# Kernel tuning notes

Hardware: AMD Instinct MI355X
Metric: run time of the kernel (lower is better)

The kernel has to match this reference:

```python
import jax, jax.numpy as jnp
import numpy as np
from jax import lax

B, T, K = 2048, 1024, 8  # batch, max seq len, num_tags


def setup_inputs() -> dict:
    key = jax.random.key(0)
    k1, k2, k3, k4, k5, k6, k7 = jax.random.split(key, 7)
    score = jax.random.normal(k1, (B, T, K), jnp.float32)
    log_p = jax.nn.log_softmax(jax.random.normal(k2, (B, T, K), jnp.float32), axis=-1)
    tags = jax.random.randint(k3, (B, T), 0, K)
    seq_l = jax.random.randint(k4, (B,), 1, T + 1)  # valid lengths in [1, T]
    transitions = jax.random.normal(k5, (K, K), jnp.float32) * 0.1
    start_transitions = jax.random.normal(k6, (K,), jnp.float32) * 0.1
    end_transitions = jax.random.normal(k7, (K,), jnp.float32) * 0.1
    return {
        "log_p": log_p,
        "score": score,
        "transitions": transitions,
        "start_transitions": start_transitions,
        "end_transitions": end_transitions,
        "tags": tags,
        "seq_l": seq_l,
    }


def _crf_nll(score, tags, mask, transitions, start_transitions, end_transitions):
    """Linear-chain CRF negative log-likelihood, summed over the batch.
    score: [B,T,K] emissions; tags: [B,T] gold; mask: [B,T] bool."""
    maskf = mask.astype(score.dtype)

    # ---- numerator: score of the gold tag path ----
    emit = jnp.take_along_axis(score, tags[..., None], axis=-1)[..., 0]  # [B,T]
    num = (emit * maskf).sum(-1)
    num = num + start_transitions[tags[:, 0]]
    trans_sc = transitions[tags[:, :-1], tags[:, 1:]]  # [B,T-1]
    num = num + (trans_sc * maskf[:, 1:]).sum(-1)
    last_idx = (mask.sum(-1).astype(jnp.int32) - 1)  # [B]
    last_tag = jnp.take_along_axis(tags, last_idx[:, None], axis=1)[:, 0]
    num = num + end_transitions[last_tag]

    # ---- denominator: log partition via log-sum-exp scan over time ----
    alpha0 = start_transitions[None, :] + score[:, 0]  # [B,K]

    def step(alpha, xs):
        emit_t, mask_t = xs  # [B,K], [B]
        # alpha[b,i] + transitions[i,j] + emit[b,j], logsumexp over i
        nxt = jax.nn.logsumexp(alpha[:, :, None] + transitions[None, :, :], axis=1) + emit_t
        alpha = jnp.where(mask_t[:, None], nxt, alpha)  # freeze past end-of-seq
        return alpha, None

    xs = (jnp.swapaxes(score[:, 1:], 0, 1), jnp.swapaxes(mask[:, 1:], 0, 1))
    alpha, _ = lax.scan(step, alpha0, xs)
    log_z = jax.nn.logsumexp(alpha + end_transitions[None, :], axis=-1)  # [B]

    return -(num - log_z).sum()


def reference(log_p, score, transitions, start_transitions, end_transitions, tags, seq_l):
    mask = jnp.arange(T)[None, :] < seq_l[:, None]  # [B,T] bool
    loss = _crf_nll(score, tags, mask, transitions, start_transitions, end_transitions) / B
    # training path: quick predictions = argmax over per-token log_p, zero-padded
    pred_idx = jnp.argmax(log_p, axis=-1) * mask.astype(jnp.int64)
    return loss, pred_idx
```

## Files before the change

### kernel.cpp

```cpp
#include <hip/hip_runtime.h>
#include <hip/hip_bf16.h>


namespace {

constexpr int B = 2048;
constexpr int T = 1024;

__device__ __forceinline__ float max8(const float* a) {
  return fmaxf(fmaxf(fmaxf(a[0], a[1]), fmaxf(a[2], a[3])),
               fmaxf(fmaxf(a[4], a[5]), fmaxf(a[6], a[7])));
}

__global__ __launch_bounds__(256) void pred_num_kernel(
    const float* __restrict__ log_p, const float* __restrict__ score,
    const float* __restrict__ trans, const float* __restrict__ start_tr,
    const float* __restrict__ end_tr, const int* __restrict__ tags,
    const int* __restrict__ seq_l, float* __restrict__ out_pred,
    float* __restrict__ ws_num) {
  int tid = blockIdx.x * blockDim.x + threadIdx.x;
  int g0 = tid << 2;
  int b = g0 >> 10;
  int t0 = g0 & (T - 1);
  int L = seq_l[b];

  const float4* lp = reinterpret_cast<const float4*>(log_p) + (g0 << 1);
  float4 u[8];
#pragma unroll
  for (int r = 0; r < 8; ++r) u[r] = lp[r];
  int4 tg4 = *reinterpret_cast<const int4*>(tags + g0);
  int tg[4] = {tg4.x, tg4.y, tg4.z, tg4.w};
  int prev0 = (t0 == 0) ? 0 : tags[g0 - 1];

  float contrib = 0.0f;
#pragma unroll
  for (int r = 0; r < 4; ++r) {
    float v[8] = {u[2 * r].x, u[2 * r].y, u[2 * r].z, u[2 * r].w,
                  u[2 * r + 1].x, u[2 * r + 1].y, u[2 * r + 1].z,
                  u[2 * r + 1].w};
    int best = 0;
    float bv = v[0];
#pragma unroll
    for (int j = 1; j < 8; ++j) {
      if (v[j] > bv) { bv = v[j]; best = j; }
    }
    int t = t0 + r;
    bool act = (t < L);
    out_pred[g0 + r] = act ? (float)best : 0.0f;
    if (act) {
      int tgr = tg[r];
      float csum = score[(size_t)(g0 + r) * 8 + tgr];
      if (t == 0)
        csum += start_tr[tgr];
      else
        csum += trans[((r == 0) ? prev0 : tg[r - 1]) * 8 + tgr];
      if (t == L - 1) csum += end_tr[tgr];
      contrib += csum;
    }
  }
#pragma unroll
  for (int off = 32; off >= 1; off >>= 1) contrib += __shfl_down(contrib, off);
  if ((threadIdx.x & 63) == 0) atomicAdd(&ws_num[b], contrib);
}

template <int NC, int LOG_NC>
__global__ __launch_bounds__(256) void chunk_kernel(
    const float* __restrict__ score, const float* __restrict__ trans,
    const int* __restrict__ seq_l, float* __restrict__ wsA,
    float* __restrict__ wsS) {
  constexpr int CL = T / NC;
  int g = blockIdx.x * blockDim.x + threadIdx.x;
  int k = g & 7;
  int c = (g >> 3) & (NC - 1);
  int b = g >> (3 + LOG_NC);

  float E[8][8];
#pragma unroll
  for (int i = 0; i < 8; ++i)
#pragma unroll
    for (int j = 0; j < 8; ++j) E[i][j] = __expf(trans[i * 8 + j]);

  float a[8];
#pragma unroll
  for (int j = 0; j < 8; ++j) a[j] = (j == k) ? 1.0f : 0.0f;
  float sig = 0.0f;

  int L = seq_l[b];
  int t0 = c * CL;
  int ts = (c == 0) ? 1 : t0;
  int te = min(t0 + CL, L);
  int n = te - ts;
  const float* sp = score + ((size_t)b * T + ts) * 8;

  float4 nA, nB;
  if (n > 0) {
    nA = *reinterpret_cast<const float4*>(sp);
    nB = *reinterpret_cast<const float4*>(sp + 4);
  }
  for (int it = 0; it < n; ++it) {
    float4 sA = nA, sB = nB;
    if (it + 1 < n) {
      nA = *reinterpret_cast<const float4*>(sp + 8);
      nB = *reinterpret_cast<const float4*>(sp + 12);
    }
    sp += 8;
    float em[8] = {__expf(sA.x), __expf(sA.y), __expf(sA.z), __expf(sA.w),
                   __expf(sB.x), __expf(sB.y), __expf(sB.z), __expf(sB.w)};
    float na[8];
#pragma unroll
    for (int j = 0; j < 8; ++j) {
      float acc = E[0][j] * a[0];
#pragma unroll
      for (int i = 1; i < 8; ++i) acc = fmaf(E[i][j], a[i], acc);
      na[j] = em[j] * acc;
    }
#pragma unroll
    for (int j = 0; j < 8; ++j) a[j] = na[j];
    if ((it & 7) == 7) {
      float mm = max8(a);
      float r = __builtin_amdgcn_rcpf(mm);
#pragma unroll
      for (int j = 0; j < 8; ++j) a[j] *= r;
      sig += __logf(mm);
    }
  }
  {
    float mm = max8(a);
    if (mm > 0.0f) {
      float r = __builtin_amdgcn_rcpf(mm);
#pragma unroll
      for (int j = 0; j < 8; ++j) a[j] *= r;
      sig += __logf(mm);
    }
  }

  float* Ao = wsA + (size_t)(b * NC + c) * 64;
#pragma unroll
  for (int j = 0; j < 8; ++j) Ao[j * 8 + k] = a[j];
  wsS[(b * NC + c) * 8 + k] = sig;
}

template <int NC>
__global__ __launch_bounds__(256) void combine_kernel(
    const float* __restrict__ score, const float* __restrict__ start_tr,
    const float* __restrict__ end_tr, const float* __restrict__ wsA,
    const float* __restrict__ wsS, const float* __restrict__ ws_num,
    float* __restrict__ out_loss) {
  int tid = blockIdx.x * blockDim.x + threadIdx.x;
  int j = tid & 7;
  int b = tid >> 3;

  float pj = __expf(start_tr[j] + score[(size_t)b * T * 8 + j]);
  float mm = pj;
#pragma unroll
  for (int m = 1; m < 8; m <<= 1) mm = fmaxf(mm, __shfl_xor(mm, m, 8));
  float tau = __logf(mm);
  pj *= __builtin_amdgcn_rcpf(mm);

  float eej = __expf(end_tr[j]);

  const float* Ab = wsA + (size_t)b * NC * 64;
  const float* Sb = wsS + (size_t)b * NC * 8;
  float4 r0 = *reinterpret_cast<const float4*>(Ab + j * 8);
  float4 r1 = *reinterpret_cast<const float4*>(Ab + j * 8 + 4);
  float sgj = Sb[j];

  for (int c = 0; c < NC; ++c) {
    float4 c0 = r0, c1 = r1;
    float sj = sgj;
    if (c + 1 < NC) {
      const float* An = Ab + (size_t)(c + 1) * 64;
      r0 = *reinterpret_cast<const float4*>(An + j * 8);
      r1 = *reinterpret_cast<const float4*>(An + j * 8 + 4);
      sgj = Sb[(c + 1) * 8 + j];
    }
    float smax = sj;
#pragma unroll
    for (int m = 1; m < 8; m <<= 1) smax = fmaxf(smax, __shfl_xor(smax, m, 8));
    float wj = pj * __expf(sj - smax);
    float w[8];
#pragma unroll
    for (int i = 0; i < 8; ++i) w[i] = __shfl(wj, i, 8);
    float acc = c0.x * w[0];
    acc = fmaf(c0.y, w[1], acc);
    acc = fmaf(c0.z, w[2], acc);
    acc = fmaf(c0.w, w[3], acc);
    acc = fmaf(c1.x, w[4], acc);
    acc = fmaf(c1.y, w[5], acc);
    acc = fmaf(c1.z, w[6], acc);
    acc = fmaf(c1.w, w[7], acc);
    float mm2 = acc;
#pragma unroll
    for (int m = 1; m < 8; m <<= 1) mm2 = fmaxf(mm2, __shfl_xor(mm2, m, 8));
    tau += smax + __logf(mm2);
    pj = acc * __builtin_amdgcn_rcpf(mm2);
  }

  float term = pj * eej;
#pragma unroll
  for (int m = 1; m < 8; m <<= 1) term += __shfl_xor(term, m, 8);
  float logz = tau + __logf(term);

  float part = (j == 0) ? (logz - ws_num[b]) * (1.0f / (float)B) : 0.0f;
#pragma unroll
  for (int off = 32; off >= 1; off >>= 1) part += __shfl_down(part, off);
  if ((threadIdx.x & 63) == 0) atomicAdd(out_loss, part);
}

}

extern "C" void kernel_launch(void* const* d_in, const int* in_sizes, int n_in,
                              void* d_out, int out_size, void* d_ws,
                              size_t ws_size, hipStream_t stream) {
  const float* log_p = (const float*)d_in[0];
  const float* score = (const float*)d_in[1];
  const float* trans = (const float*)d_in[2];
  const float* start_tr = (const float*)d_in[3];
  const float* end_tr = (const float*)d_in[4];
  const int* tags = (const int*)d_in[5];
  const int* seq_l = (const int*)d_in[6];
  float* out = (float*)d_out;

  size_t need64 = ((size_t)B * 64 * 72 + B) * sizeof(float);
  bool use64 = ws_size >= need64;

  int nc = use64 ? 64 : 32;
  float* wsA = (float*)d_ws;
  float* wsS = wsA + (size_t)B * nc * 64;
  float* wsNum = wsS + (size_t)B * nc * 8;

  hipMemsetAsync(wsNum, 0, B * sizeof(float), stream);
  hipMemsetAsync(out, 0, sizeof(float), stream);

  pred_num_kernel<<<(B * T / 4) / 256, 256, 0, stream>>>(
      log_p, score, trans, start_tr, end_tr, tags, seq_l, out + 1, wsNum);
  if (use64) {
    chunk_kernel<64, 6><<<(B * 64 * 8) / 256, 256, 0, stream>>>(
        score, trans, seq_l, wsA, wsS);
    combine_kernel<64><<<(B * 8) / 256, 256, 0, stream>>>(
        score, start_tr, end_tr, wsA, wsS, wsNum, out);
  } else {
    chunk_kernel<32, 5><<<(B * 32 * 8) / 256, 256, 0, stream>>>(
        score, trans, seq_l, wsA, wsS);
    combine_kernel<32><<<(B * 8) / 256, 256, 0, stream>>>(
        score, start_tr, end_tr, wsA, wsS, wsNum, out);
  }
}
```

Baseline: 236.7 us.

## Balance CRF chunks by sequence length, use persistent work queue and tree combine

Chunks are now sized by each sequence's valid length, so every chunk does similar work and no chunk runs past the end of a sequence. A persistent grid pulls tasks from an atomic counter. Score loads are cooperative float4 reads, with the emissions spread to lanes by shuffles. The serial per-batch combine over 64 chunks becomes a log-depth tree reduction of transfer matrices in shared memory, one block per batch. The exp of the transition matrix is computed once in an init kernel, which also replaces the memsets, and the workspace-size fallback is removed, so the workspace must be large enough.

```diff
diff --git a/kernel.cpp b/kernel.cpp
--- a/kernel.cpp
+++ b/kernel.cpp
@@ -6,10 +6,23 @@
 
 constexpr int B = 2048;
 constexpr int T = 1024;
+constexpr int NC = 64;
+constexpr int NTASK = B * (NC / 8);
 
 __device__ __forceinline__ float max8(const float* a) {
   return fmaxf(fmaxf(fmaxf(a[0], a[1]), fmaxf(a[2], a[3])),
                fmaxf(fmaxf(a[4], a[5]), fmaxf(a[6], a[7])));
+}
+
+__global__ void init_kernel(const float* __restrict__ trans,
+                            float* __restrict__ expE,
+                            float* __restrict__ ws_num, int* __restrict__ ctr,
+                            float* __restrict__ out0) {
+  int i = threadIdx.x;
+  for (int r = i; r < B; r += 256) ws_num[r] = 0.0f;
+  if (i < 64) expE[i] = __expf(trans[i]);
+  if (i == 64) *ctr = 0;
+  if (i == 65) *out0 = 0.0f;
 }
 
 __global__ __launch_bounds__(256) void pred_num_kernel(
@@ -63,148 +76,191 @@
   if ((threadIdx.x & 63) == 0) atomicAdd(&ws_num[b], contrib);
 }
 
-template <int NC, int LOG_NC>
 __global__ __launch_bounds__(256) void chunk_kernel(
-    const float* __restrict__ score, const float* __restrict__ trans,
+    const float* __restrict__ score, const float* __restrict__ expE,
     const int* __restrict__ seq_l, float* __restrict__ wsA,
-    float* __restrict__ wsS) {
-  constexpr int CL = T / NC;
-  int g = blockIdx.x * blockDim.x + threadIdx.x;
-  int k = g & 7;
-  int c = (g >> 3) & (NC - 1);
-  int b = g >> (3 + LOG_NC);
-
-  float E[8][8];
-#pragma unroll
-  for (int i = 0; i < 8; ++i)
-#pragma unroll
-    for (int j = 0; j < 8; ++j) E[i][j] = __expf(trans[i * 8 + j]);
-
-  float a[8];
-#pragma unroll
-  for (int j = 0; j < 8; ++j) a[j] = (j == k) ? 1.0f : 0.0f;
-  float sig = 0.0f;
-
-  int L = seq_l[b];
-  int t0 = c * CL;
-  int ts = (c == 0) ? 1 : t0;
-  int te = min(t0 + CL, L);
-  int n = te - ts;
-  const float* sp = score + ((size_t)b * T + ts) * 8;
-
-  float4 nA, nB;
-  if (n > 0) {
-    nA = *reinterpret_cast<const float4*>(sp);
-    nB = *reinterpret_cast<const float4*>(sp + 4);
-  }
-  for (int it = 0; it < n; ++it) {
-    float4 sA = nA, sB = nB;
-    if (it + 1 < n) {
-      nA = *reinterpret_cast<const float4*>(sp + 8);
-      nB = *reinterpret_cast<const float4*>(sp + 12);
-    }
-    sp += 8;
-    float em[8] = {__expf(sA.x), __expf(sA.y), __expf(sA.z), __expf(sA.w),
-                   __expf(sB.x), __expf(sB.y), __expf(sB.z), __expf(sB.w)};
-    float na[8];
-#pragma unroll
-    for (int j = 0; j < 8; ++j) {
-      float acc = E[0][j] * a[0];
-#pragma unroll
-      for (int i = 1; i < 8; ++i) acc = fmaf(E[i][j], a[i], acc);
-      na[j] = em[j] * acc;
-    }
-#pragma unroll
-    for (int j = 0; j < 8; ++j) a[j] = na[j];
-    if ((it & 7) == 7) {
+    float* __restrict__ wsS, int* __restrict__ ctr) {
+  float E[64];
+#pragma unroll
+  for (int i = 0; i < 64; ++i) E[i] = expE[i];
+
+  int lane = threadIdx.x & 63;
+  int grp = lane >> 3;
+  int k = lane & 7;
+
+  for (;;) {
+    int tv = 0;
+    if (lane == 0) tv = atomicAdd(ctr, 1);
+    int task = __shfl(tv, 0);
+    if (task >= NTASK) break;
+    int b = task >> 3;
+    int oct = task & 7;
+    int c = oct * 8 + grp;
+
+    int S = seq_l[b] - 1;
+    int ts = 1 + ((S * c) >> 6);
+    int te = 1 + ((S * (c + 1)) >> 6);
+    int nblk = (te - ts + 3) >> 2;
+
+    float a[8];
+#pragma unroll
+    for (int j = 0; j < 8; ++j) a[j] = (j == k) ? 1.0f : 0.0f;
+    float sig = 0.0f;
+
+    const float* rowb = score + (size_t)b * T * 8;
+    int t = ts;
+    float4 cur;
+    if (nblk > 0) {
+      int tl = min(t + (k >> 1), T - 1);
+      cur = *reinterpret_cast<const float4*>(rowb + tl * 8 + (k & 1) * 4);
+    }
+    for (int blk = 0; blk < nblk; ++blk) {
+      float4 nxt = cur;
+      if (blk + 1 < nblk) {
+        int tl = min(t + 4 + (k >> 1), T - 1);
+        nxt = *reinterpret_cast<const float4*>(rowb + tl * 8 + (k & 1) * 4);
+      }
+      float4 ex = make_float4(__expf(cur.x), __expf(cur.y), __expf(cur.z),
+                              __expf(cur.w));
+      int nst = min(4, te - t);
+#pragma unroll
+      for (int s = 0; s < 4; ++s) {
+        if (s >= nst) break;
+        float em[8];
+        em[0] = __shfl(ex.x, 2 * s, 8);
+        em[1] = __shfl(ex.y, 2 * s, 8);
+        em[2] = __shfl(ex.z, 2 * s, 8);
+        em[3] = __shfl(ex.w, 2 * s, 8);
+        em[4] = __shfl(ex.x, 2 * s + 1, 8);
+        em[5] = __shfl(ex.y, 2 * s + 1, 8);
+        em[6] = __shfl(ex.z, 2 * s + 1, 8);
+        em[7] = __shfl(ex.w, 2 * s + 1, 8);
+        float na[8];
+#pragma unroll
+        for (int j = 0; j < 8; ++j) {
+          float acc = E[0 * 8 + j] * a[0];
+#pragma unroll
+          for (int i = 1; i < 8; ++i) acc = fmaf(E[i * 8 + j], a[i], acc);
+          na[j] = em[j] * acc;
+        }
+#pragma unroll
+        for (int j = 0; j < 8; ++j) a[j] = na[j];
+      }
+      if (blk & 1) {
+        float mm = max8(a);
+        float r = __builtin_amdgcn_rcpf(mm);
+#pragma unroll
+        for (int j = 0; j < 8; ++j) a[j] *= r;
+        sig += __logf(mm);
+      }
+      cur = nxt;
+      t += 4;
+    }
+    {
       float mm = max8(a);
-      float r = __builtin_amdgcn_rcpf(mm);
-#pragma unroll
-      for (int j = 0; j < 8; ++j) a[j] *= r;
-      sig += __logf(mm);
-    }
-  }
-  {
-    float mm = max8(a);
-    if (mm > 0.0f) {
-      float r = __builtin_amdgcn_rcpf(mm);
-#pragma unroll
-      for (int j = 0; j < 8; ++j) a[j] *= r;
-      sig += __logf(mm);
-    }
-  }
-
-  float* Ao = wsA + (size_t)(b * NC + c) * 64;
-#pragma unroll
-  for (int j = 0; j < 8; ++j) Ao[j * 8 + k] = a[j];
-  wsS[(b * NC + c) * 8 + k] = sig;
-}
-
-template <int NC>
+      if (mm > 0.0f) {
+        float r = __builtin_amdgcn_rcpf(mm);
+#pragma unroll
+        for (int j = 0; j < 8; ++j) a[j] *= r;
+        sig += __logf(mm);
+      }
+    }
+
+    float* Ao = wsA + (size_t)(b * NC + c) * 64;
+#pragma unroll
+    for (int j = 0; j < 8; ++j) Ao[j * 8 + k] = a[j];
+    wsS[(b * NC + c) * 8 + k] = sig;
+  }
+}
+
 __global__ __launch_bounds__(256) void combine_kernel(
     const float* __restrict__ score, const float* __restrict__ start_tr,
     const float* __restrict__ end_tr, const float* __restrict__ wsA,
     const float* __restrict__ wsS, const float* __restrict__ ws_num,
     float* __restrict__ out_loss) {
-  int tid = blockIdx.x * blockDim.x + threadIdx.x;
-  int j = tid & 7;
-  int b = tid >> 3;
-
-  float pj = __expf(start_tr[j] + score[(size_t)b * T * 8 + j]);
-  float mm = pj;
-#pragma unroll
-  for (int m = 1; m < 8; m <<= 1) mm = fmaxf(mm, __shfl_xor(mm, m, 8));
-  float tau = __logf(mm);
-  pj *= __builtin_amdgcn_rcpf(mm);
-
-  float eej = __expf(end_tr[j]);
-
+  __shared__ float sm[96 * 73];
+  int b = blockIdx.x;
+  int tid = threadIdx.x;
   const float* Ab = wsA + (size_t)b * NC * 64;
   const float* Sb = wsS + (size_t)b * NC * 8;
-  float4 r0 = *reinterpret_cast<const float4*>(Ab + j * 8);
-  float4 r1 = *reinterpret_cast<const float4*>(Ab + j * 8 + 4);
-  float sgj = Sb[j];
-
-  for (int c = 0; c < NC; ++c) {
-    float4 c0 = r0, c1 = r1;
-    float sj = sgj;
-    if (c + 1 < NC) {
-      const float* An = Ab + (size_t)(c + 1) * 64;
-      r0 = *reinterpret_cast<const float4*>(An + j * 8);
-      r1 = *reinterpret_cast<const float4*>(An + j * 8 + 4);
-      sgj = Sb[(c + 1) * 8 + j];
-    }
-    float smax = sj;
-#pragma unroll
-    for (int m = 1; m < 8; m <<= 1) smax = fmaxf(smax, __shfl_xor(smax, m, 8));
-    float wj = pj * __expf(sj - smax);
-    float w[8];
-#pragma unroll
-    for (int i = 0; i < 8; ++i) w[i] = __shfl(wj, i, 8);
-    float acc = c0.x * w[0];
-    acc = fmaf(c0.y, w[1], acc);
-    acc = fmaf(c0.z, w[2], acc);
-    acc = fmaf(c0.w, w[3], acc);
-    acc = fmaf(c1.x, w[4], acc);
-    acc = fmaf(c1.y, w[5], acc);
-    acc = fmaf(c1.z, w[6], acc);
-    acc = fmaf(c1.w, w[7], acc);
-    float mm2 = acc;
-#pragma unroll
-    for (int m = 1; m < 8; m <<= 1) mm2 = fmaxf(mm2, __shfl_xor(mm2, m, 8));
-    tau += smax + __logf(mm2);
-    pj = acc * __builtin_amdgcn_rcpf(mm2);
-  }
-
-  float term = pj * eej;
-#pragma unroll
-  for (int m = 1; m < 8; m <<= 1) term += __shfl_xor(term, m, 8);
-  float logz = tau + __logf(term);
-
-  float part = (j == 0) ? (logz - ws_num[b]) * (1.0f / (float)B) : 0.0f;
-#pragma unroll
-  for (int off = 32; off >= 1; off >>= 1) part += __shfl_down(part, off);
-  if ((threadIdx.x & 63) == 0) atomicAdd(out_loss, part);
+
+#pragma unroll
+  for (int r = 0; r < 4; ++r) {
+    int vi = tid + r * 256;
+    int g = vi * 4;
+    int c = g >> 6, rem = g & 63;
+    float4 q = reinterpret_cast<const float4*>(Ab)[vi];
+    float* dst = &sm[c * 73 + rem];
+    dst[0] = q.x; dst[1] = q.y; dst[2] = q.z; dst[3] = q.w;
+  }
+#pragma unroll
+  for (int r = 0; r < 2; ++r) {
+    int gi = tid + r * 256;
+    sm[(gi >> 3) * 73 + 64 + (gi & 7)] = Sb[gi];
+  }
+  __syncthreads();
+
+  float* bufB = &sm[64 * 73];
+  int p = tid >> 3, k = tid & 7;
+#pragma unroll
+  for (int lvl = 1; lvl <= 6; ++lvl) {
+    int nprod = NC >> lvl;
+    float* inb = (lvl & 1) ? sm : bufB;
+    float* outb = (lvl & 1) ? bufB : sm;
+    if (p < nprod) {
+      const float* M0 = inb + (size_t)(2 * p) * 73;
+      const float* M1 = inb + (size_t)(2 * p + 1) * 73;
+      float s1[8];
+#pragma unroll
+      for (int i = 0; i < 8; ++i) s1[i] = M1[64 + i];
+      float m = max8(s1);
+      float w[8];
+#pragma unroll
+      for (int i = 0; i < 8; ++i) w[i] = M0[i * 8 + k] * __expf(s1[i] - m);
+      float u[8];
+#pragma unroll
+      for (int j = 0; j < 8; ++j) {
+        float acc = M1[j * 8 + 0] * w[0];
+#pragma unroll
+        for (int i = 1; i < 8; ++i) acc = fmaf(M1[j * 8 + i], w[i], acc);
+        u[j] = acc;
+      }
+      float mm = fmaxf(max8(u), 1e-37f);
+      float rc = __builtin_amdgcn_rcpf(mm);
+      float* D = outb + (size_t)p * 73;
+#pragma unroll
+      for (int j = 0; j < 8; ++j) D[j * 8 + k] = u[j] * rc;
+      D[64 + k] = M0[64 + k] + m + __logf(mm);
+    }
+    __syncthreads();
+  }
+
+  if (tid < 8) {
+    int j = tid;
+    float p0 = __expf(start_tr[j] + score[(size_t)b * T * 8 + j]);
+    float m0 = p0;
+#pragma unroll
+    for (int m = 1; m < 8; m <<= 1) m0 = fmaxf(m0, __shfl_xor(m0, m, 8));
+    float p0n = p0 * __builtin_amdgcn_rcpf(m0);
+    float p0a[8];
+#pragma unroll
+    for (int i = 0; i < 8; ++i) p0a[i] = __shfl(p0n, i, 8);
+    float sM[8];
+#pragma unroll
+    for (int i = 0; i < 8; ++i) sM[i] = sm[64 + i];
+    float mS = max8(sM);
+    float inner = 0.0f;
+#pragma unroll
+    for (int i = 0; i < 8; ++i)
+      inner = fmaf(sm[j * 8 + i], __expf(sM[i] - mS) * p0a[i], inner);
+    float term = inner * __expf(end_tr[j]);
+#pragma unroll
+    for (int m = 1; m < 8; m <<= 1) term += __shfl_xor(term, m, 8);
+    if (j == 0) {
+      float logz = __logf(m0) + mS + __logf(term);
+      atomicAdd(out_loss, (logz - ws_num[b]) * (1.0f / (float)B));
+    }
+  }
 }
 
 }
@@ -221,28 +277,17 @@
   const int* seq_l = (const int*)d_in[6];
   float* out = (float*)d_out;
 
-  size_t need64 = ((size_t)B * 64 * 72 + B) * sizeof(float);
-  bool use64 = ws_size >= need64;
-
-  int nc = use64 ? 64 : 32;
   float* wsA = (float*)d_ws;
-  float* wsS = wsA + (size_t)B * nc * 64;
-  float* wsNum = wsS + (size_t)B * nc * 8;
-
-  hipMemsetAsync(wsNum, 0, B * sizeof(float), stream);
-  hipMemsetAsync(out, 0, sizeof(float), stream);
-
+  float* wsS = wsA + (size_t)B * NC * 64;
+  float* wsNum = wsS + (size_t)B * NC * 8;
+  float* wsExpE = wsNum + B;
+  int* wsCtr = (int*)(wsExpE + 64);
+
+  init_kernel<<<1, 256, 0, stream>>>(trans, wsExpE, wsNum, wsCtr, out);
   pred_num_kernel<<<(B * T / 4) / 256, 256, 0, stream>>>(
       log_p, score, trans, start_tr, end_tr, tags, seq_l, out + 1, wsNum);
-  if (use64) {
-    chunk_kernel<64, 6><<<(B * 64 * 8) / 256, 256, 0, stream>>>(
-        score, trans, seq_l, wsA, wsS);
-    combine_kernel<64><<<(B * 8) / 256, 256, 0, stream>>>(
-        score, start_tr, end_tr, wsA, wsS, wsNum, out);
-  } else {
-    chunk_kernel<32, 5><<<(B * 32 * 8) / 256, 256, 0, stream>>>(
-        score, trans, seq_l, wsA, wsS);
-    combine_kernel<32><<<(B * 8) / 256, 256, 0, stream>>>(
-        score, start_tr, end_tr, wsA, wsS, wsNum, out);
-  }
-}
+  chunk_kernel<<<1024, 256, 0, stream>>>(score, wsExpE, seq_l, wsA, wsS,
+                                         wsCtr);
+  combine_kernel<<<B, 256, 0, stream>>>(score, start_tr, end_tr, wsA, wsS,
+                                        wsNum, out);
+}
```

After: 438.3 us. 1.85x slower.
